# Kernel optimization log

Measured on AMD Instinct MI355X. Metric: run time of the kernel, lower is better.

Reference implementation:

```python
import jax, jax.numpy as jnp
import numpy as np

AGENT, WIN = 6, 7
HEADS, DIM_HEAD = 8, 32
SCALE = DIM_HEAD ** -0.5
N = AGENT * WIN * WIN  # 294 tokens per window


def _rel_pos_index():
    # static Swin-3D relative position index, computed once in numpy
    coords = np.stack(np.meshgrid(np.arange(AGENT), np.arange(WIN), np.arange(WIN), indexing='ij'))
    flat = coords.reshape(3, -1)                      # [3, N]
    rel = flat[:, :, None] - flat[:, None, :]        # [3, N, N]
    rel = rel.transpose(1, 2, 0).copy()              # [N, N, 3]
    rel[..., 0] += AGENT - 1
    rel[..., 1] += WIN - 1
    rel[..., 2] += WIN - 1
    rel[..., 0] *= (2 * WIN - 1) * (2 * WIN - 1)
    rel[..., 1] *= 2 * WIN - 1
    return jnp.asarray(rel.sum(-1))                  # [N, N] int

RPI = _rel_pos_index()


def setup_inputs() -> dict:
    key = jax.random.key(0)
    k1, k2, k3, k4 = jax.random.split(key, 4)
    dim = 256
    x = jax.random.normal(k1, (1, AGENT, 16, 16, WIN, WIN, dim), dtype=jnp.float32)
    w_qkv = jax.random.normal(k2, (3 * HEADS * DIM_HEAD, dim), dtype=jnp.float32) * 0.02
    w_out = jax.random.normal(k3, (dim, HEADS * DIM_HEAD), dtype=jnp.float32) * 0.02
    n_bias = (2 * AGENT - 1) * (2 * WIN - 1) * (2 * WIN - 1)  # 1859
    bias_table = jax.random.normal(k4, (n_bias, HEADS), dtype=jnp.float32) * 0.02
    return {"x": x, "w_qkv": w_qkv, "w_out": w_out, "bias_table": bias_table}


def reference(x, w_qkv, w_out, bias_table):
    b, l, hx, wy, w1, w2, d = x.shape
    # 'b l x y w1 w2 d -> (b x y) (l w1 w2) d'
    xw = jnp.transpose(x, (0, 2, 3, 1, 4, 5, 6)).reshape(b * hx * wy, l * w1 * w2, d)
    qkv = xw @ w_qkv.T                                # [B, N, 3*h*dh]
    q, k, v = jnp.split(qkv, 3, axis=-1)
    def heads(t):
        B, n, _ = t.shape
        return t.reshape(B, n, HEADS, DIM_HEAD).transpose(0, 2, 1, 3)  # [B, h, N, dh]
    q, k, v = heads(q) * SCALE, heads(k), heads(v)
    sim = jnp.einsum('bhid,bhjd->bhij', q, k)        # [B, h, N, N]
    bias = bias_table[RPI]                            # [N, N, h]
    sim = sim + jnp.transpose(bias, (2, 0, 1))[None]  # broadcast over B
    attn = jax.nn.softmax(sim, axis=-1)
    out = jnp.einsum('bhij,bhjd->bhid', attn, v)      # [B, h, N, dh]
    B = b * hx * wy
    out = out.transpose(0, 2, 1, 3).reshape(B, l, w1, w2, HEADS * DIM_HEAD)
    out = out @ w_out.T                               # [B, l, w1, w2, d]
    out = out.reshape(b, hx, wy, l, w1, w2, d)
    return jnp.transpose(out, (0, 3, 1, 2, 4, 5, 6))  # b l x y w1 w2 d
```

## Files before the change

kernel.cpp:

```cpp
#include <hip/hip_runtime.h>
#include <hip/hip_bf16.h>

typedef unsigned short u16;
typedef unsigned int u32;
typedef __bf16 bf16x8_t __attribute__((ext_vector_type(8)));
typedef float fx4 __attribute__((ext_vector_type(4)));
typedef float fx16 __attribute__((ext_vector_type(16)));
typedef u16 u16x8_t __attribute__((ext_vector_type(8)));
typedef u32 u32x2_t __attribute__((ext_vector_type(2)));
typedef u32 u32x4_t __attribute__((ext_vector_type(4)));

#define QSCALE 0.25500276676267216f
#define LOG2E 1.4426950408889634f

__device__ __forceinline__ u16 f2bu(float f) {
  __bf16 h = (__bf16)f;
  return __builtin_bit_cast(u16, h);
}
__device__ __forceinline__ float bu2f(u16 b) {
  return __builtin_bit_cast(float, (u32)b << 16);
}
__device__ __forceinline__ void plswap(u32& a, u32& b) {
  u32x2_t r = __builtin_amdgcn_permlane32_swap(a, b, false, false);
  a = r[0]; b = r[1];
}

#define GLD16(gp, lp) __builtin_amdgcn_global_load_lds( \
    (const __attribute__((address_space(1))) void*)(gp), \
    (__attribute__((address_space(3))) void*)(lp), 16, 0, 0)

__global__ void prep_w(const float* __restrict__ wqkv, const float* __restrict__ wout,
                       u16* __restrict__ bqkv, u16* __restrict__ bwout) {
  int t = blockIdx.x * 256 + threadIdx.x;
  if (t < 196608) {
    float v = wqkv[t];
    if (t < 65536) v *= QSCALE;
    bqkv[t] = f2bu(v);
  } else {
    int i = t - 196608;
    bwout[i] = f2bu(wout[i]);
  }
}

__global__ void prep_bias(const float* __restrict__ table, u16* __restrict__ bias_pre) {
  int t = blockIdx.x * 256 + threadIdx.x;
  int lane = t & 63;
  int rest = t >> 6;
  int tile = rest % 10; rest /= 10;
  int s = rest % 10; int h = rest / 10;
  int q = s * 32 + (lane & 31); if (q > 293) q = 293;
  int l1 = q / 49, r1 = q % 49, a1 = r1 / 7, b1 = r1 % 7;
  u16x8_t o0, o1;
#pragma unroll
  for (int r = 0; r < 16; ++r) {
    int key = tile * 32 + (r & 3) + 8 * (r >> 2) + 4 * (lane >> 5);
    float v;
    if (key >= 294) {
      v = -1e30f;
    } else {
      int l2 = key / 49, r2 = key % 49, a2 = r2 / 7, b2 = r2 % 7;
      int idx = (l1 - l2 + 5) * 169 + (a1 - a2 + 6) * 13 + (b1 - b2 + 6);
      v = table[idx * 8 + h] * LOG2E;
    }
    if (r < 8) o0[r] = f2bu(v); else o1[r - 8] = f2bu(v);
  }
  u16* dst = bias_pre + (size_t)t * 16;
  *(u16x8_t*)(dst) = o0;
  *(u16x8_t*)(dst + 8) = o1;
}

__global__ __launch_bounds__(256, 2) void gemm_qkv(const float* __restrict__ X,
                                                   const u16* __restrict__ Bw,
                                                   u16* __restrict__ C) {
  __shared__ u16 sA[128 * 32];
  __shared__ u16 sB[128 * 32];
  const int tid = threadIdx.x, lane = tid & 63, wave = tid >> 6;
  const int wr = wave >> 1, wc = wave & 1;
  const int tm = blockIdx.x, tn = blockIdx.y;
  size_t xb[2];
#pragma unroll
  for (int rnd = 0; rnd < 2; ++rnd) {
    int row = rnd * 64 + (tid >> 2);
    int m = tm * 128 + row;
    int b = m / 294, n = m % 294;
    int hx = b >> 4, wy = b & 15;
    int l = n / 49, rem = n % 49, w1 = rem / 7, w2 = rem % 7;
    xb[rnd] = (((((size_t)l * 16 + hx) * 16 + wy) * 7 + w1) * 7 + w2) * 256 + (tid & 3) * 8;
  }
  fx4 acc[4][4] = {};
#pragma unroll 1
  for (int kt = 0; kt < 8; ++kt) {
    __syncthreads();
#pragma unroll
    for (int rnd = 0; rnd < 2; ++rnd) {
      int o = rnd * 4096 + tid * 16;
      const float4* src = (const float4*)(X + xb[rnd] + kt * 32);
      float4 v0 = src[0], v1 = src[1];
      u16x8_t a8;
      a8[0] = f2bu(v0.x); a8[1] = f2bu(v0.y); a8[2] = f2bu(v0.z); a8[3] = f2bu(v0.w);
      a8[4] = f2bu(v1.x); a8[5] = f2bu(v1.y); a8[6] = f2bu(v1.z); a8[7] = f2bu(v1.w);
      *(u16x8_t*)((char*)sA + o) = a8;
      int row = o >> 6, cb = o & 63;
      const u16* gB = Bw + (size_t)(tn * 128 + row) * 256 + kt * 32 + (cb >> 1);
      GLD16(gB, (char*)sB + o);
    }
    __syncthreads();
    bf16x8_t af[4], bfr[4];
#pragma unroll
    for (int i = 0; i < 4; ++i)
      af[i] = *(const bf16x8_t*)&sA[(wr * 64 + i * 16 + (lane & 15)) * 32 + (lane >> 4) * 8];
#pragma unroll
    for (int j = 0; j < 4; ++j)
      bfr[j] = *(const bf16x8_t*)&sB[(wc * 64 + j * 16 + (lane & 15)) * 32 + (lane >> 4) * 8];
#pragma unroll
    for (int i = 0; i < 4; ++i)
#pragma unroll
      for (int j = 0; j < 4; ++j)
        acc[i][j] = __builtin_amdgcn_mfma_f32_16x16x32_bf16(af[i], bfr[j], acc[i][j], 0, 0, 0);
  }
  const int r0 = tm * 128 + wr * 64, c0 = tn * 128 + wc * 64;
#pragma unroll
  for (int i = 0; i < 4; ++i)
#pragma unroll
    for (int j = 0; j < 4; ++j)
#pragma unroll
      for (int r = 0; r < 4; ++r) {
        int row = r0 + i * 16 + (lane >> 4) * 4 + r;
        int col = c0 + j * 16 + (lane & 15);
        C[(size_t)row * 768 + col] = f2bu(acc[i][j][r]);
      }
}

__global__ __launch_bounds__(256, 2) void gemm_proj(const u16* __restrict__ A,
                                                    const u16* __restrict__ Bw,
                                                    float* __restrict__ Cf) {
  __shared__ u16 sA[128 * 32];
  __shared__ u16 sB[128 * 32];
  const int tid = threadIdx.x, lane = tid & 63, wave = tid >> 6;
  const int wr = wave >> 1, wc = wave & 1;
  const int tm = blockIdx.x, tn = blockIdx.y;
  fx4 acc[4][4] = {};
#pragma unroll 1
  for (int kt = 0; kt < 8; ++kt) {
    __syncthreads();
#pragma unroll
    for (int rnd = 0; rnd < 2; ++rnd) {
      int o = rnd * 4096 + tid * 16;
      int row = o >> 6, cb = o & 63;
      const u16* gA = A + (size_t)(tm * 128 + row) * 256 + kt * 32 + (cb >> 1);
      const u16* gB = Bw + (size_t)(tn * 128 + row) * 256 + kt * 32 + (cb >> 1);
      GLD16(gA, (char*)sA + o);
      GLD16(gB, (char*)sB + o);
    }
    __syncthreads();
    bf16x8_t af[4], bfr[4];
#pragma unroll
    for (int i = 0; i < 4; ++i)
      af[i] = *(const bf16x8_t*)&sA[(wr * 64 + i * 16 + (lane & 15)) * 32 + (lane >> 4) * 8];
#pragma unroll
    for (int j = 0; j < 4; ++j)
      bfr[j] = *(const bf16x8_t*)&sB[(wc * 64 + j * 16 + (lane & 15)) * 32 + (lane >> 4) * 8];
#pragma unroll
    for (int i = 0; i < 4; ++i)
#pragma unroll
      for (int j = 0; j < 4; ++j)
        acc[i][j] = __builtin_amdgcn_mfma_f32_16x16x32_bf16(af[i], bfr[j], acc[i][j], 0, 0, 0);
  }
  const int r0 = tm * 128 + wr * 64, c0 = tn * 128 + wc * 64;
#pragma unroll
  for (int i = 0; i < 4; ++i)
#pragma unroll
    for (int j = 0; j < 4; ++j)
#pragma unroll
      for (int r = 0; r < 4; ++r) {
        int row = r0 + i * 16 + (lane >> 4) * 4 + r;
        int col = c0 + j * 16 + (lane & 15);
        int b = row / 294, n = row % 294;
        int hx = b >> 4, wy = b & 15;
        int l = n / 49, rem = n % 49, w1 = rem / 7, w2 = rem % 7;
        size_t off = (((((size_t)l * 16 + hx) * 16 + wy) * 7 + w1) * 7 + w2) * 256 + col;
        Cf[off] = acc[i][j][r];
      }
}

__device__ __forceinline__ int vt_byte(int d, int tok) {
  return d * 656 + ((d >> 3) & 3) * 32 + tok * 2;
}

__global__ __launch_bounds__(256, 4) void attn(const u16* __restrict__ qkv,
                                               const u16* __restrict__ bias_pre,
                                               u16* __restrict__ aout) {
  __shared__ __align__(16) u16 VT[10560];
  const int blk = blockIdx.x;
  const int b = blk >> 3, h = blk & 7;
  const int tid = threadIdx.x, lane = tid & 63, wave = tid >> 6;
  const int l31 = lane & 31, g5 = lane >> 5;
  const size_t base = (size_t)b * 294 * 768;

  for (int i = tid; i < 1280; i += 256) {
    int tok = i >> 2, c8 = (i & 3) * 8;
    u16x8_t v;
    if (tok < 294) {
      v = *(const u16x8_t*)(qkv + base + (size_t)tok * 768 + 512 + h * 32 + c8);
    } else {
#pragma unroll
      for (int j = 0; j < 8; ++j) v[j] = 0;
    }
#pragma unroll
    for (int j = 0; j < 8; ++j)
      *(u16*)((char*)VT + vt_byte(c8 + j, tok)) = v[j];
  }
  __syncthreads();

#pragma unroll 1
  for (int s = wave; s < 10; s += 4) {
    int qr = s * 32 + l31; if (qr > 293) qr = 293;
    const u16* qb = qkv + base + (size_t)qr * 768 + h * 32 + g5 * 8;
    bf16x8_t qf0 = *(const bf16x8_t*)(qb);
    bf16x8_t qf1 = *(const bf16x8_t*)(qb + 16);

    fx16 O;
#pragma unroll
    for (int r = 0; r < 16; ++r) O[r] = 0.f;
    float sv = 0.f;
    const u16* bp = bias_pre + ((size_t)((h * 10 + s) * 10) * 64 + lane) * 16;
    int kr = l31;

#pragma unroll 1
    for (int t = 0; t < 10; ++t) {
      u16x8_t b0 = *(const u16x8_t*)(bp + t * 1024);
      u16x8_t b1 = *(const u16x8_t*)(bp + t * 1024 + 8);
      fx16 a;
#pragma unroll
      for (int j = 0; j < 8; ++j) { a[j] = bu2f(b0[j]); a[8 + j] = bu2f(b1[j]); }
      int krc = kr > 293 ? 293 : kr;
      const u16* kb = qkv + base + (size_t)krc * 768 + 256 + h * 32 + g5 * 8;
      bf16x8_t kf0 = *(const bf16x8_t*)(kb);
      bf16x8_t kf1 = *(const bf16x8_t*)(kb + 16);
      a = __builtin_amdgcn_mfma_f32_32x32x16_bf16(kf0, qf0, a, 0, 0, 0);
      a = __builtin_amdgcn_mfma_f32_32x32x16_bf16(kf1, qf1, a, 0, 0, 0);
      kr += 32;
      u32 pk[8];
#pragma unroll
      for (int j = 0; j < 8; ++j) {
        float e0 = __builtin_exp2f(a[2 * j]);
        float e1 = __builtin_exp2f(a[2 * j + 1]);
        sv += e0 + e1;
        pk[j] = (u32)f2bu(e0) | ((u32)f2bu(e1) << 16);
      }
#pragma unroll
      for (int kh = 0; kh < 2; ++kh) {
        u32 w0 = pk[kh * 4 + 0], w1 = pk[kh * 4 + 1];
        u32 w2 = pk[kh * 4 + 2], w3 = pk[kh * 4 + 3];
        plswap(w0, w2);
        plswap(w1, w3);
        u32x4_t w; w[0] = w0; w[1] = w1; w[2] = w2; w[3] = w3;
        bf16x8_t pf = __builtin_bit_cast(bf16x8_t, w);
        bf16x8_t vf = *(const bf16x8_t*)((char*)VT + vt_byte(l31, t * 32 + kh * 16 + g5 * 8));
        O = __builtin_amdgcn_mfma_f32_32x32x16_bf16(pf, vf, O, 0, 0, 0);
      }
    }

    sv += __shfl_xor(sv, 32);
    float inv = 1.0f / sv;

#pragma unroll
    for (int r = 0; r < 16; ++r) {
      int qrow = (r & 3) + 8 * (r >> 2) + 4 * g5;
      int qo = s * 32 + qrow;
      if (qo < 294) {
        float iv = __shfl(inv, qrow);
        aout[((size_t)b * 294 + qo) * 256 + h * 32 + l31] = f2bu(O[r] * iv);
      }
    }
  }
}

extern "C" void kernel_launch(void* const* d_in, const int* in_sizes, int n_in,
                              void* d_out, int out_size, void* d_ws, size_t ws_size,
                              hipStream_t stream) {
  (void)in_sizes; (void)n_in; (void)out_size; (void)ws_size;
  const float* x    = (const float*)d_in[0];
  const float* wqkv = (const float*)d_in[1];
  const float* wout = (const float*)d_in[2];
  const float* btab = (const float*)d_in[3];
  float* out = (float*)d_out;
  char* ws = (char*)d_ws;
  u16* aout  = (u16*)(ws);
  u16* bqkv  = (u16*)(ws + 38535168);
  u16* bwout = (u16*)(ws + 38928384);
  u16* biasp = (u16*)(ws + 39059456);
  u16* qkv   = (u16*)(ws + 40697856);

  prep_w<<<1024, 256, 0, stream>>>(wqkv, wout, bqkv, bwout);
  prep_bias<<<200, 256, 0, stream>>>(btab, biasp);
  gemm_qkv<<<dim3(588, 6), 256, 0, stream>>>(x, bqkv, qkv);
  attn<<<2048, 256, 0, stream>>>(qkv, biasp, aout);
  gemm_proj<<<dim3(588, 2), 256, 0, stream>>>(aout, bwout, out);
}
```

Before: 334.2 us.

## Store QKV head-major, use 5 waves with two query tiles each sharing K/V loads

The QKV GEMM now writes its output in a [window, q/k/v, head, token, dim] layout, so each attention block reads Q, K and V as contiguous per-head slabs instead of strided 768-wide rows. The attention kernel launches 320 threads (5 waves), and each wave handles two query tiles. K and V fragments are loaded once per key tile and reused for both query tiles. The relative-position bias is precomputed in fp32 instead of bf16, which removes the unpack step but doubles the bias bytes read, and the launch bound drops its occupancy hint.

```diff
diff --git a/kernel.cpp b/kernel.cpp
--- a/kernel.cpp
+++ b/kernel.cpp
@@ -16,9 +16,6 @@
 __device__ __forceinline__ u16 f2bu(float f) {
   __bf16 h = (__bf16)f;
   return __builtin_bit_cast(u16, h);
-}
-__device__ __forceinline__ float bu2f(u16 b) {
-  return __builtin_bit_cast(float, (u32)b << 16);
 }
 __device__ __forceinline__ void plswap(u32& a, u32& b) {
   u32x2_t r = __builtin_amdgcn_permlane32_swap(a, b, false, false);
@@ -42,7 +39,7 @@
   }
 }
 
-__global__ void prep_bias(const float* __restrict__ table, u16* __restrict__ bias_pre) {
+__global__ void prep_bias(const float* __restrict__ table, float* __restrict__ bias_pre) {
   int t = blockIdx.x * 256 + threadIdx.x;
   int lane = t & 63;
   int rest = t >> 6;
@@ -50,7 +47,7 @@
   int s = rest % 10; int h = rest / 10;
   int q = s * 32 + (lane & 31); if (q > 293) q = 293;
   int l1 = q / 49, r1 = q % 49, a1 = r1 / 7, b1 = r1 % 7;
-  u16x8_t o0, o1;
+  fx4 o[4];
 #pragma unroll
   for (int r = 0; r < 16; ++r) {
     int key = tile * 32 + (r & 3) + 8 * (r >> 2) + 4 * (lane >> 5);
@@ -62,11 +59,11 @@
       int idx = (l1 - l2 + 5) * 169 + (a1 - a2 + 6) * 13 + (b1 - b2 + 6);
       v = table[idx * 8 + h] * LOG2E;
     }
-    if (r < 8) o0[r] = f2bu(v); else o1[r - 8] = f2bu(v);
-  }
-  u16* dst = bias_pre + (size_t)t * 16;
-  *(u16x8_t*)(dst) = o0;
-  *(u16x8_t*)(dst + 8) = o1;
+    o[r >> 2][r & 3] = v;
+  }
+  float* dst = bias_pre + (size_t)t * 16;
+#pragma unroll
+  for (int q4 = 0; q4 < 4; ++q4) *(fx4*)(dst + q4 * 4) = o[q4];
 }
 
 __global__ __launch_bounds__(256, 2) void gemm_qkv(const float* __restrict__ X,
@@ -127,7 +124,9 @@
       for (int r = 0; r < 4; ++r) {
         int row = r0 + i * 16 + (lane >> 4) * 4 + r;
         int col = c0 + j * 16 + (lane & 15);
-        C[(size_t)row * 768 + col] = f2bu(acc[i][j][r]);
+        int bwin = row / 294, n = row % 294;
+        int sel = col >> 8, hh = (col >> 5) & 7, d = col & 31;
+        C[((((size_t)bwin * 3 + sel) * 8 + hh) * 294 + n) * 32 + d] = f2bu(acc[i][j][r]);
       }
 }
 
@@ -187,21 +186,23 @@
   return d * 656 + ((d >> 3) & 3) * 32 + tok * 2;
 }
 
-__global__ __launch_bounds__(256, 4) void attn(const u16* __restrict__ qkv,
-                                               const u16* __restrict__ bias_pre,
-                                               u16* __restrict__ aout) {
+__global__ __launch_bounds__(320) void attn(const u16* __restrict__ qkv2,
+                                            const float* __restrict__ bias_pre,
+                                            u16* __restrict__ aout) {
   __shared__ __align__(16) u16 VT[10560];
   const int blk = blockIdx.x;
   const int b = blk >> 3, h = blk & 7;
   const int tid = threadIdx.x, lane = tid & 63, wave = tid >> 6;
   const int l31 = lane & 31, g5 = lane >> 5;
-  const size_t base = (size_t)b * 294 * 768;
-
-  for (int i = tid; i < 1280; i += 256) {
+  const u16* qb_ = qkv2 + ((size_t)(b * 3 + 0) * 8 + h) * 294 * 32;
+  const u16* kb_ = qkv2 + ((size_t)(b * 3 + 1) * 8 + h) * 294 * 32;
+  const u16* vb_ = qkv2 + ((size_t)(b * 3 + 2) * 8 + h) * 294 * 32;
+
+  for (int i = tid; i < 1280; i += 320) {
     int tok = i >> 2, c8 = (i & 3) * 8;
     u16x8_t v;
     if (tok < 294) {
-      v = *(const u16x8_t*)(qkv + base + (size_t)tok * 768 + 512 + h * 32 + c8);
+      v = *(const u16x8_t*)(vb_ + tok * 32 + c8);
     } else {
 #pragma unroll
       for (int j = 0; j < 8; ++j) v[j] = 0;
@@ -212,67 +213,105 @@
   }
   __syncthreads();
 
+  const int s0 = wave, s1 = wave + 5;
+  int qr0 = s0 * 32 + l31; if (qr0 > 293) qr0 = 293;
+  int qr1 = s1 * 32 + l31; if (qr1 > 293) qr1 = 293;
+  const u16* q0p = qb_ + qr0 * 32;
+  const u16* q1p = qb_ + qr1 * 32;
+  bf16x8_t qa0 = *(const bf16x8_t*)(q0p + g5 * 8);
+  bf16x8_t qa1 = *(const bf16x8_t*)(q0p + 16 + g5 * 8);
+  bf16x8_t qb0 = *(const bf16x8_t*)(q1p + g5 * 8);
+  bf16x8_t qb1 = *(const bf16x8_t*)(q1p + 16 + g5 * 8);
+
+  fx16 O0, O1;
+#pragma unroll
+  for (int r = 0; r < 16; ++r) { O0[r] = 0.f; O1[r] = 0.f; }
+  float sva0 = 0.f, svb0 = 0.f, sva1 = 0.f, svb1 = 0.f;
+  const float* bp0 = bias_pre + ((size_t)(h * 10 + s0) * 10) * 1024 + lane * 16;
+  const float* bp1 = bias_pre + ((size_t)(h * 10 + s1) * 10) * 1024 + lane * 16;
+
 #pragma unroll 1
-  for (int s = wave; s < 10; s += 4) {
-    int qr = s * 32 + l31; if (qr > 293) qr = 293;
-    const u16* qb = qkv + base + (size_t)qr * 768 + h * 32 + g5 * 8;
-    bf16x8_t qf0 = *(const bf16x8_t*)(qb);
-    bf16x8_t qf1 = *(const bf16x8_t*)(qb + 16);
-
-    fx16 O;
-#pragma unroll
-    for (int r = 0; r < 16; ++r) O[r] = 0.f;
-    float sv = 0.f;
-    const u16* bp = bias_pre + ((size_t)((h * 10 + s) * 10) * 64 + lane) * 16;
-    int kr = l31;
-
-#pragma unroll 1
-    for (int t = 0; t < 10; ++t) {
-      u16x8_t b0 = *(const u16x8_t*)(bp + t * 1024);
-      u16x8_t b1 = *(const u16x8_t*)(bp + t * 1024 + 8);
+  for (int t = 0; t < 10; ++t) {
+    int krc = t * 32 + l31; if (krc > 293) krc = 293;
+    const u16* kp = kb_ + krc * 32;
+    bf16x8_t kf0 = *(const bf16x8_t*)(kp + g5 * 8);
+    bf16x8_t kf1 = *(const bf16x8_t*)(kp + 16 + g5 * 8);
+    bf16x8_t vf0 = *(const bf16x8_t*)((char*)VT + vt_byte(l31, t * 32 + g5 * 8));
+    bf16x8_t vf1 = *(const bf16x8_t*)((char*)VT + vt_byte(l31, t * 32 + 16 + g5 * 8));
+
+    {
+      const float* bp = bp0 + t * 1024;
       fx16 a;
 #pragma unroll
-      for (int j = 0; j < 8; ++j) { a[j] = bu2f(b0[j]); a[8 + j] = bu2f(b1[j]); }
-      int krc = kr > 293 ? 293 : kr;
-      const u16* kb = qkv + base + (size_t)krc * 768 + 256 + h * 32 + g5 * 8;
-      bf16x8_t kf0 = *(const bf16x8_t*)(kb);
-      bf16x8_t kf1 = *(const bf16x8_t*)(kb + 16);
-      a = __builtin_amdgcn_mfma_f32_32x32x16_bf16(kf0, qf0, a, 0, 0, 0);
-      a = __builtin_amdgcn_mfma_f32_32x32x16_bf16(kf1, qf1, a, 0, 0, 0);
-      kr += 32;
+      for (int q4 = 0; q4 < 4; ++q4) {
+        fx4 bv = *(const fx4*)(bp + q4 * 4);
+        a[q4 * 4 + 0] = bv[0]; a[q4 * 4 + 1] = bv[1];
+        a[q4 * 4 + 2] = bv[2]; a[q4 * 4 + 3] = bv[3];
+      }
+      a = __builtin_amdgcn_mfma_f32_32x32x16_bf16(kf0, qa0, a, 0, 0, 0);
+      a = __builtin_amdgcn_mfma_f32_32x32x16_bf16(kf1, qa1, a, 0, 0, 0);
       u32 pk[8];
 #pragma unroll
       for (int j = 0; j < 8; ++j) {
         float e0 = __builtin_exp2f(a[2 * j]);
         float e1 = __builtin_exp2f(a[2 * j + 1]);
-        sv += e0 + e1;
+        sva0 += e0; svb0 += e1;
         pk[j] = (u32)f2bu(e0) | ((u32)f2bu(e1) << 16);
       }
-#pragma unroll
-      for (int kh = 0; kh < 2; ++kh) {
-        u32 w0 = pk[kh * 4 + 0], w1 = pk[kh * 4 + 1];
-        u32 w2 = pk[kh * 4 + 2], w3 = pk[kh * 4 + 3];
-        plswap(w0, w2);
-        plswap(w1, w3);
-        u32x4_t w; w[0] = w0; w[1] = w1; w[2] = w2; w[3] = w3;
-        bf16x8_t pf = __builtin_bit_cast(bf16x8_t, w);
-        bf16x8_t vf = *(const bf16x8_t*)((char*)VT + vt_byte(l31, t * 32 + kh * 16 + g5 * 8));
-        O = __builtin_amdgcn_mfma_f32_32x32x16_bf16(pf, vf, O, 0, 0, 0);
-      }
-    }
-
-    sv += __shfl_xor(sv, 32);
-    float inv = 1.0f / sv;
-
-#pragma unroll
-    for (int r = 0; r < 16; ++r) {
-      int qrow = (r & 3) + 8 * (r >> 2) + 4 * g5;
-      int qo = s * 32 + qrow;
-      if (qo < 294) {
-        float iv = __shfl(inv, qrow);
-        aout[((size_t)b * 294 + qo) * 256 + h * 32 + l31] = f2bu(O[r] * iv);
-      }
-    }
+      u32 w0 = pk[0], w1 = pk[1], w2 = pk[2], w3 = pk[3];
+      plswap(w0, w2); plswap(w1, w3);
+      u32x4_t wv; wv[0] = w0; wv[1] = w1; wv[2] = w2; wv[3] = w3;
+      O0 = __builtin_amdgcn_mfma_f32_32x32x16_bf16(__builtin_bit_cast(bf16x8_t, wv), vf0, O0, 0, 0, 0);
+      u32 y0 = pk[4], y1 = pk[5], y2 = pk[6], y3 = pk[7];
+      plswap(y0, y2); plswap(y1, y3);
+      u32x4_t yv; yv[0] = y0; yv[1] = y1; yv[2] = y2; yv[3] = y3;
+      O0 = __builtin_amdgcn_mfma_f32_32x32x16_bf16(__builtin_bit_cast(bf16x8_t, yv), vf1, O0, 0, 0, 0);
+    }
+    {
+      const float* bp = bp1 + t * 1024;
+      fx16 a;
+#pragma unroll
+      for (int q4 = 0; q4 < 4; ++q4) {
+        fx4 bv = *(const fx4*)(bp + q4 * 4);
+        a[q4 * 4 + 0] = bv[0]; a[q4 * 4 + 1] = bv[1];
+        a[q4 * 4 + 2] = bv[2]; a[q4 * 4 + 3] = bv[3];
+      }
+      a = __builtin_amdgcn_mfma_f32_32x32x16_bf16(kf0, qb0, a, 0, 0, 0);
+      a = __builtin_amdgcn_mfma_f32_32x32x16_bf16(kf1, qb1, a, 0, 0, 0);
+      u32 pk[8];
+#pragma unroll
+      for (int j = 0; j < 8; ++j) {
+        float e0 = __builtin_exp2f(a[2 * j]);
+        float e1 = __builtin_exp2f(a[2 * j + 1]);
+        sva1 += e0; svb1 += e1;
+        pk[j] = (u32)f2bu(e0) | ((u32)f2bu(e1) << 16);
+      }
+      u32 w0 = pk[0], w1 = pk[1], w2 = pk[2], w3 = pk[3];
+      plswap(w0, w2); plswap(w1, w3);
+      u32x4_t wv; wv[0] = w0; wv[1] = w1; wv[2] = w2; wv[3] = w3;
+      O1 = __builtin_amdgcn_mfma_f32_32x32x16_bf16(__builtin_bit_cast(bf16x8_t, wv), vf0, O1, 0, 0, 0);
+      u32 y0 = pk[4], y1 = pk[5], y2 = pk[6], y3 = pk[7];
+      plswap(y0, y2); plswap(y1, y3);
+      u32x4_t yv; yv[0] = y0; yv[1] = y1; yv[2] = y2; yv[3] = y3;
+      O1 = __builtin_amdgcn_mfma_f32_32x32x16_bf16(__builtin_bit_cast(bf16x8_t, yv), vf1, O1, 0, 0, 0);
+    }
+  }
+
+  float sv0 = sva0 + svb0; sv0 += __shfl_xor(sv0, 32);
+  float sv1 = sva1 + svb1; sv1 += __shfl_xor(sv1, 32);
+  float inv0 = 1.0f / sv0, inv1 = 1.0f / sv1;
+
+#pragma unroll
+  for (int r = 0; r < 16; ++r) {
+    int qrow = (r & 3) + 8 * (r >> 2) + 4 * g5;
+    int qo0 = s0 * 32 + qrow;
+    float iv0 = __shfl(inv0, qrow);
+    if (qo0 < 294)
+      aout[((size_t)b * 294 + qo0) * 256 + h * 32 + l31] = f2bu(O0[r] * iv0);
+    int qo1 = s1 * 32 + qrow;
+    float iv1 = __shfl(inv1, qrow);
+    if (qo1 < 294)
+      aout[((size_t)b * 294 + qo1) * 256 + h * 32 + l31] = f2bu(O1[r] * iv1);
   }
 }
 
@@ -286,15 +325,15 @@
   const float* btab = (const float*)d_in[3];
   float* out = (float*)d_out;
   char* ws = (char*)d_ws;
-  u16* aout  = (u16*)(ws);
-  u16* bqkv  = (u16*)(ws + 38535168);
-  u16* bwout = (u16*)(ws + 38928384);
-  u16* biasp = (u16*)(ws + 39059456);
-  u16* qkv   = (u16*)(ws + 40697856);
+  u16* aout   = (u16*)(ws);
+  u16* bqkv   = (u16*)(ws + 38535168);
+  u16* bwout  = (u16*)(ws + 38928384);
+  float* biasp = (float*)(ws + 39059456);
+  u16* qkv2   = (u16*)(ws + 42336256);
 
   prep_w<<<1024, 256, 0, stream>>>(wqkv, wout, bqkv, bwout);
   prep_bias<<<200, 256, 0, stream>>>(btab, biasp);
-  gemm_qkv<<<dim3(588, 6), 256, 0, stream>>>(x, bqkv, qkv);
-  attn<<<2048, 256, 0, stream>>>(qkv, biasp, aout);
+  gemm_qkv<<<dim3(588, 6), 256, 0, stream>>>(x, bqkv, qkv2);
+  attn<<<2048, 320, 0, stream>>>(qkv2, biasp, aout);
   gemm_proj<<<dim3(588, 2), 256, 0, stream>>>(aout, bwout, out);
 }
```

New measurement: 357.1 us. +6.8%, slower.
